# Kernel tuning notes

Measured on AMD Instinct MI355X. Metric: run time of the kernel, lower is better.

The kernel has to match this reference:

```python
import jax, jax.numpy as jnp
import numpy as np

SMOOTHING = 0.9  # NEURON_CONFIG['signal_smoothing']
NUM_SOURCE = 16384
NUM_TARGET = 16384
NUM_BRANCHES = 64
BATCH = 32


def setup_inputs() -> dict:
    key = jax.random.key(0)
    k1, k2, k3, k4 = jax.random.split(key, 4)
    spikes = jax.random.normal(k1, (BATCH, NUM_SOURCE), dtype=jnp.float32)
    attenuation = jax.random.uniform(k2, (NUM_SOURCE, NUM_BRANCHES), dtype=jnp.float32)
    target_indices = jax.random.randint(k3, (NUM_SOURCE, NUM_BRANCHES), 0, NUM_TARGET)
    delays = jax.random.randint(k4, (NUM_SOURCE, NUM_BRANCHES), 0, 6)
    return {"spikes": spikes, "attenuation": attenuation,
            "target_indices": target_indices, "delays": delays}


def reference(spikes, attenuation, target_indices, delays):
    # spikes: [B, S]; attenuation/delays/target_indices: [S, Br]
    B = spikes.shape[0]
    num_target = NUM_TARGET
    att = jnp.clip(attenuation, 0.0, 1.0)
    decay = SMOOTHING ** delays.astype(spikes.dtype)          # [S, Br]
    # fused elementwise: signal per (batch, source, branch)
    signals = spikes[:, :, None] * (att * decay)[None, :, :]   # [B, S, Br]
    flat_t = target_indices.reshape(-1)                        # [S*Br]
    flat_s = signals.reshape(B, -1)                            # [B, S*Br]
    out = jnp.zeros((B, num_target), dtype=spikes.dtype)
    out = out.at[jnp.arange(B)[:, None], flat_t[None, :]].add(flat_s)
    return out
```

## Files before the change

### kernel.cpp

```cpp
#include <hip/hip_runtime.h>

#define S_   16384
#define T_   16384
#define B_   32
#define NEDGES (S_ * 64)
#define GP_  512
#define EPG  2048
#define NBKT 512
#define TPB  32
#define CAP_SRT   2560
#define CAP_STASH 512

__device__ __forceinline__ float edge_weight(float a, int d) {
  float w = fminf(fmaxf(a, 0.0f), 1.0f);
  float r = (d & 1) ? 0.9f : 1.0f;
  r = (d & 2) ? r * 0.81f   : r;
  r = (d & 4) ? r * 0.6561f : r;
  return w * r;
}

__global__ __launch_bounds__(512) void produce(
    const float* __restrict__ spikes,
    const float* __restrict__ att,
    const int*   __restrict__ tgt,
    const int*   __restrict__ del,
    float*        __restrict__ spikesT,
    int2*         __restrict__ rec,
    unsigned int* __restrict__ ofse) {
  __shared__ float tile[32][33];
  __shared__ int4  sbuf4[EPG / 2];
  __shared__ int   cnt5[NBKT], cur5[NBKT], sofs5[NBKT];
  __shared__ int   wtot[8];
  int2* buf = (int2*)sbuf4;

  const int g   = blockIdx.x;
  const int tid = threadIdx.x;
  cnt5[tid] = 0;

  const int s0 = g * 32;
  {
    const int x = tid & 31, y = tid >> 5;
    tile[x][y]      = spikes[(size_t)y        * S_ + s0 + x];
    tile[x][y + 16] = spikes[(size_t)(y + 16) * S_ + s0 + x];
  }

  const int e4  = g * 512 + tid;
  int4   t = reinterpret_cast<const int4*>(tgt)[e4];
  float4 a = reinterpret_cast<const float4*>(att)[e4];
  int4   d = reinterpret_cast<const int4*>(del)[e4];
  const int src = e4 >> 4;

  __syncthreads();

  {
    const int b = tid & 31, j = tid >> 5;
    spikesT[(size_t)(s0 + j)      * 32 + b] = tile[j][b];
    spikesT[(size_t)(s0 + j + 16) * 32 + b] = tile[j + 16][b];
  }

  const int bk0 = t.x >> 5, bk1 = t.y >> 5, bk2 = t.z >> 5, bk3 = t.w >> 5;
  __hip_atomic_fetch_add(&cnt5[bk0], 1, __ATOMIC_RELAXED, __HIP_MEMORY_SCOPE_WORKGROUP);
  __hip_atomic_fetch_add(&cnt5[bk1], 1, __ATOMIC_RELAXED, __HIP_MEMORY_SCOPE_WORKGROUP);
  __hip_atomic_fetch_add(&cnt5[bk2], 1, __ATOMIC_RELAXED, __HIP_MEMORY_SCOPE_WORKGROUP);
  __hip_atomic_fetch_add(&cnt5[bk3], 1, __ATOMIC_RELAXED, __HIP_MEMORY_SCOPE_WORKGROUP);
  __syncthreads();

  int v = cnt5[tid];
  int incl = v;
#pragma unroll
  for (int off = 1; off < 64; off <<= 1) {
    int u = __shfl_up(incl, off);
    if ((tid & 63) >= off) incl += u;
  }
  if ((tid & 63) == 63) wtot[tid >> 6] = incl;
  __syncthreads();
  {
    int base = 0;
    const int wv = tid >> 6;
    for (int i = 0; i < wv; ++i) base += wtot[i];
    const int start = base + incl - v;
    sofs5[tid] = start;
    cur5[tid]  = start;
  }
  __syncthreads();

#define PUT(BK, TL, AV, DV)                                                   \
  {                                                                           \
    int p = __hip_atomic_fetch_add(&cur5[BK], 1, __ATOMIC_RELAXED,            \
                                   __HIP_MEMORY_SCOPE_WORKGROUP);             \
    buf[p] = make_int2(((TL) << 14) | src,                                    \
                       __float_as_int(edge_weight((AV), (DV))));              \
  }
  PUT(bk0, t.x & 31, a.x, d.x)
  PUT(bk1, t.y & 31, a.y, d.y)
  PUT(bk2, t.z & 31, a.z, d.z)
  PUT(bk3, t.w & 31, a.w, d.w)
#undef PUT
  __syncthreads();

  int4* recO = reinterpret_cast<int4*>(rec) + (size_t)g * (EPG / 2);
  recO[tid]       = sbuf4[tid];
  recO[tid + 512] = sbuf4[tid + 512];
  ofse[(size_t)g * NBKT + tid] =
      ((unsigned)cur5[tid] << 16) | (unsigned)sofs5[tid];
}

__global__ __launch_bounds__(256) void transpose_ofse(
    const unsigned int* __restrict__ in, unsigned int* __restrict__ out) {
  __shared__ unsigned tl[32][33];
  const int x = threadIdx.x, y = threadIdx.y;
  const int r0 = blockIdx.y * 32, c0 = blockIdx.x * 32;
  for (int i = y; i < 32; i += 8)
    tl[i][x] = in[(size_t)(r0 + i) * NBKT + c0 + x];
  __syncthreads();
  for (int i = y; i < 32; i += 8)
    out[(size_t)(c0 + i) * GP_ + r0 + x] = tl[x][i];
}

__global__ __launch_bounds__(512) void consume(
    const int2*  __restrict__ rec,
    const unsigned int* __restrict__ ofseT,
    const float* __restrict__ spikesT,
    float* __restrict__ out) {
  __shared__ int2  srt[CAP_SRT];
  __shared__ int2  stash[CAP_STASH];
  __shared__ float otile[TPB][33];
  __shared__ unsigned sse[GP_];
  __shared__ int   h32[TPB], ofs[TPB + 1], cur32[TPB];
  __shared__ int   stash_n;

  const int k   = blockIdx.x;
  const int tid = threadIdx.x;
  const int b   = tid & 31;
  const int hw  = tid >> 5;
  const int sub = (b >> 3);
  const int j   = b & 7;

  if (tid < TPB) h32[tid] = 0;
  if (tid == 0)  stash_n = 0;
  sse[tid] = ofseT[(size_t)k * GP_ + tid];
  __syncthreads();

  int2 rr[8];
  int  rv = 0;
#pragma unroll
  for (int it = 0; it < 8; ++it) {
    const int g = it * 64 + hw * 4 + sub;
    const unsigned u = sse[g];
    const int st = (int)(u & 0xFFFF);
    const int n  = (int)(u >> 16) - st;
    const int2* slice = rec + (size_t)g * EPG + st;
    if (j < n) {
      int2 r = slice[j];
      __hip_atomic_fetch_add(&h32[(r.x >> 14) & 31], 1, __ATOMIC_RELAXED,
                             __HIP_MEMORY_SCOPE_WORKGROUP);
      rr[it] = r;
      rv |= 1 << it;
    }
    for (int j2 = j + 8; j2 < n; j2 += 8) {
      int2 r = slice[j2];
      __hip_atomic_fetch_add(&h32[(r.x >> 14) & 31], 1, __ATOMIC_RELAXED,
                             __HIP_MEMORY_SCOPE_WORKGROUP);
      int sp = __hip_atomic_fetch_add(&stash_n, 1, __ATOMIC_RELAXED,
                                      __HIP_MEMORY_SCOPE_WORKGROUP);
      if (sp < CAP_STASH) stash[sp] = r;
    }
  }
  __syncthreads();

  if (tid < 32) {
    int vv = h32[tid], ii = vv;
#pragma unroll
    for (int off = 1; off < 32; off <<= 1) {
      int uu = __shfl_up(ii, off);
      if (tid >= off) ii += uu;
    }
    ofs[tid]   = ii - vv;
    cur32[tid] = ii - vv;
    if (tid == 31) ofs[32] = ii;
  }
  __syncthreads();

#pragma unroll
  for (int it = 0; it < 8; ++it)
    if (rv & (1 << it)) {
      int2 r = rr[it];
      int p = __hip_atomic_fetch_add(&cur32[(r.x >> 14) & 31], 1,
                                     __ATOMIC_RELAXED,
                                     __HIP_MEMORY_SCOPE_WORKGROUP);
      if (p < CAP_SRT) srt[p] = r;
    }
  const int ns = min(stash_n, CAP_STASH);
  for (int i = tid; i < ns; i += 512) {
    int2 r = stash[i];
    int p = __hip_atomic_fetch_add(&cur32[(r.x >> 14) & 31], 1,
                                   __ATOMIC_RELAXED,
                                   __HIP_MEMORY_SCOPE_WORKGROUP);
    if (p < CAP_SRT) srt[p] = r;
  }
  __syncthreads();

  float acc0 = 0.f, acc1 = 0.f;
  {
    int e        = ofs[hw];
    const int e1 = min(ofs[hw + 1], CAP_SRT);
    for (; e + 4 <= e1; e += 4) {
      int2 r0 = srt[e], r1 = srt[e + 1], r2 = srt[e + 2], r3 = srt[e + 3];
      float s0 = spikesT[(size_t)(r0.x & 0x3FFF) * 32 + b];
      float s1 = spikesT[(size_t)(r1.x & 0x3FFF) * 32 + b];
      float s2 = spikesT[(size_t)(r2.x & 0x3FFF) * 32 + b];
      float s3 = spikesT[(size_t)(r3.x & 0x3FFF) * 32 + b];
      acc0 = fmaf(__int_as_float(r0.y), s0, acc0);
      acc0 = fmaf(__int_as_float(r1.y), s1, acc0);
      acc0 = fmaf(__int_as_float(r2.y), s2, acc0);
      acc0 = fmaf(__int_as_float(r3.y), s3, acc0);
    }
    for (; e < e1; ++e) {
      int2 r = srt[e];
      acc0 = fmaf(__int_as_float(r.y), spikesT[(size_t)(r.x & 0x3FFF) * 32 + b], acc0);
    }
  }
  {
    int e        = ofs[hw + 16];
    const int e1 = min(ofs[hw + 17], CAP_SRT);
    for (; e + 4 <= e1; e += 4) {
      int2 r0 = srt[e], r1 = srt[e + 1], r2 = srt[e + 2], r3 = srt[e + 3];
      float s0 = spikesT[(size_t)(r0.x & 0x3FFF) * 32 + b];
      float s1 = spikesT[(size_t)(r1.x & 0x3FFF) * 32 + b];
      float s2 = spikesT[(size_t)(r2.x & 0x3FFF) * 32 + b];
      float s3 = spikesT[(size_t)(r3.x & 0x3FFF) * 32 + b];
      acc1 = fmaf(__int_as_float(r0.y), s0, acc1);
      acc1 = fmaf(__int_as_float(r1.y), s1, acc1);
      acc1 = fmaf(__int_as_float(r2.y), s2, acc1);
      acc1 = fmaf(__int_as_float(r3.y), s3, acc1);
    }
    for (; e < e1; ++e) {
      int2 r = srt[e];
      acc1 = fmaf(__int_as_float(r.y), spikesT[(size_t)(r.x & 0x3FFF) * 32 + b], acc1);
    }
  }

  otile[hw][b]      = acc0;
  otile[hw + 16][b] = acc1;
  __syncthreads();
  const int bb = tid >> 4;
  const int cc = (tid & 15) * 2;
  float2 o2 = make_float2(otile[cc][bb], otile[cc + 1][bb]);
  *reinterpret_cast<float2*>(&out[(size_t)bb * T_ + k * 32 + cc]) = o2;
}

__global__ void zero_floats(float* __restrict__ p, int n) {
  int i = blockIdx.x * blockDim.x + threadIdx.x;
  if (i < n) p[i] = 0.0f;
}

__global__ void naive_kernel(const float* __restrict__ spikes,
                             const float* __restrict__ att,
                             const int*   __restrict__ tgt,
                             const int*   __restrict__ del,
                             float*       __restrict__ out) {
  int i = blockIdx.x * blockDim.x + threadIdx.x;
  if (i >= NEDGES) return;
  int   s = i >> 6;
  int   t = tgt[i];
  float w = edge_weight(att[i], del[i]);
  for (int b = 0; b < B_; ++b)
    unsafeAtomicAdd(&out[(size_t)b * T_ + t], w * spikes[(size_t)b * S_ + s]);
}

extern "C" void kernel_launch(void* const* d_in, const int* in_sizes, int n_in,
                              void* d_out, int out_size, void* d_ws, size_t ws_size,
                              hipStream_t stream) {
  const float* spikes = (const float*)d_in[0];
  const float* att    = (const float*)d_in[1];
  const int*   tgt    = (const int*)d_in[2];
  const int*   del    = (const int*)d_in[3];
  float*       out    = (float*)d_out;

  const size_t spikesT_bytes = (size_t)S_ * B_ * sizeof(float);
  const size_t rec_bytes     = (size_t)NEDGES * sizeof(int2);
  const size_t ofse_bytes    = (size_t)GP_ * NBKT * sizeof(unsigned);
  const size_t need = spikesT_bytes + rec_bytes + 2 * ofse_bytes + 64;

  if (ws_size < need) {
    zero_floats<<<(B_ * T_ + 255) / 256, 256, 0, stream>>>(out, B_ * T_);
    naive_kernel<<<(NEDGES + 255) / 256, 256, 0, stream>>>(spikes, att, tgt, del, out);
    return;
  }

  char* p = (char*)d_ws;
  float*        spikesT = (float*)p;        p += spikesT_bytes;
  int2*         rec     = (int2*)p;         p += rec_bytes;
  unsigned int* ofse    = (unsigned int*)p; p += ofse_bytes;
  unsigned int* ofseT   = (unsigned int*)p;

  produce<<<GP_, 512, 0, stream>>>(spikes, att, tgt, del, spikesT, rec, ofse);
  transpose_ofse<<<dim3(NBKT / 32, GP_ / 32), dim3(32, 8), 0, stream>>>(ofse, ofseT);
  consume<<<NBKT, 512, 0, stream>>>(rec, ofseT, spikesT, out);
}
```

Measured before the change: 94.21 us.

## Replace consume-side local sort with shared-memory atomic accumulation, drop transpose kernel

The consume kernel no longer builds a per-target histogram, prefix sum and local sort of records before accumulating. Each wavefront now walks its producer-group slices and adds weight*spike products directly into a shared 32x33 accumulator with LDS float atomics. The separate transpose kernel is removed, and consume reads the offset table with strided loads instead. This removes a kernel launch, two sort passes and several barriers, but relies on LDS float atomics, which can contend when edges in a wave share a target. It also serialises each slice's records per wave instead of spreading them across lanes.

After: 251.6 us. 2.67x slower.

```diff
diff --git a/kernel.cpp b/kernel.cpp
--- a/kernel.cpp
+++ b/kernel.cpp
@@ -8,8 +8,6 @@
 #define EPG  2048
 #define NBKT 512
 #define TPB  32
-#define CAP_SRT   2560
-#define CAP_STASH 512
 
 __device__ __forceinline__ float edge_weight(float a, int d) {
   float w = fminf(fmaxf(a, 0.0f), 1.0f);
@@ -105,147 +103,41 @@
       ((unsigned)cur5[tid] << 16) | (unsigned)sofs5[tid];
 }
 
-__global__ __launch_bounds__(256) void transpose_ofse(
-    const unsigned int* __restrict__ in, unsigned int* __restrict__ out) {
-  __shared__ unsigned tl[32][33];
-  const int x = threadIdx.x, y = threadIdx.y;
-  const int r0 = blockIdx.y * 32, c0 = blockIdx.x * 32;
-  for (int i = y; i < 32; i += 8)
-    tl[i][x] = in[(size_t)(r0 + i) * NBKT + c0 + x];
-  __syncthreads();
-  for (int i = y; i < 32; i += 8)
-    out[(size_t)(c0 + i) * GP_ + r0 + x] = tl[x][i];
-}
-
 __global__ __launch_bounds__(512) void consume(
     const int2*  __restrict__ rec,
-    const unsigned int* __restrict__ ofseT,
+    const unsigned int* __restrict__ ofse,
     const float* __restrict__ spikesT,
     float* __restrict__ out) {
-  __shared__ int2  srt[CAP_SRT];
-  __shared__ int2  stash[CAP_STASH];
-  __shared__ float otile[TPB][33];
+  __shared__ float acc[TPB][33];
   __shared__ unsigned sse[GP_];
-  __shared__ int   h32[TPB], ofs[TPB + 1], cur32[TPB];
-  __shared__ int   stash_n;
 
   const int k   = blockIdx.x;
   const int tid = threadIdx.x;
   const int b   = tid & 31;
   const int hw  = tid >> 5;
-  const int sub = (b >> 3);
-  const int j   = b & 7;
 
-  if (tid < TPB) h32[tid] = 0;
-  if (tid == 0)  stash_n = 0;
-  sse[tid] = ofseT[(size_t)k * GP_ + tid];
+  for (int i = tid; i < TPB * 33; i += 512) ((float*)acc)[i] = 0.0f;
+  sse[tid] = ofse[(size_t)tid * NBKT + k];
   __syncthreads();
 
-  int2 rr[8];
-  int  rv = 0;
-#pragma unroll
-  for (int it = 0; it < 8; ++it) {
-    const int g = it * 64 + hw * 4 + sub;
+  for (int it = 0; it < 32; ++it) {
+    const int g = hw + it * 16;
     const unsigned u = sse[g];
     const int st = (int)(u & 0xFFFF);
     const int n  = (int)(u >> 16) - st;
     const int2* slice = rec + (size_t)g * EPG + st;
-    if (j < n) {
-      int2 r = slice[j];
-      __hip_atomic_fetch_add(&h32[(r.x >> 14) & 31], 1, __ATOMIC_RELAXED,
-                             __HIP_MEMORY_SCOPE_WORKGROUP);
-      rr[it] = r;
-      rv |= 1 << it;
-    }
-    for (int j2 = j + 8; j2 < n; j2 += 8) {
-      int2 r = slice[j2];
-      __hip_atomic_fetch_add(&h32[(r.x >> 14) & 31], 1, __ATOMIC_RELAXED,
-                             __HIP_MEMORY_SCOPE_WORKGROUP);
-      int sp = __hip_atomic_fetch_add(&stash_n, 1, __ATOMIC_RELAXED,
-                                      __HIP_MEMORY_SCOPE_WORKGROUP);
-      if (sp < CAP_STASH) stash[sp] = r;
+    for (int j = 0; j < n; ++j) {
+      const int2 r = slice[j];
+      const float v = __int_as_float(r.y) *
+                      spikesT[(size_t)(r.x & 0x3FFF) * 32 + b];
+      atomicAdd(&acc[(r.x >> 14) & 31][b], v);
     }
   }
   __syncthreads();
 
-  if (tid < 32) {
-    int vv = h32[tid], ii = vv;
-#pragma unroll
-    for (int off = 1; off < 32; off <<= 1) {
-      int uu = __shfl_up(ii, off);
-      if (tid >= off) ii += uu;
-    }
-    ofs[tid]   = ii - vv;
-    cur32[tid] = ii - vv;
-    if (tid == 31) ofs[32] = ii;
-  }
-  __syncthreads();
-
-#pragma unroll
-  for (int it = 0; it < 8; ++it)
-    if (rv & (1 << it)) {
-      int2 r = rr[it];
-      int p = __hip_atomic_fetch_add(&cur32[(r.x >> 14) & 31], 1,
-                                     __ATOMIC_RELAXED,
-                                     __HIP_MEMORY_SCOPE_WORKGROUP);
-      if (p < CAP_SRT) srt[p] = r;
-    }
-  const int ns = min(stash_n, CAP_STASH);
-  for (int i = tid; i < ns; i += 512) {
-    int2 r = stash[i];
-    int p = __hip_atomic_fetch_add(&cur32[(r.x >> 14) & 31], 1,
-                                   __ATOMIC_RELAXED,
-                                   __HIP_MEMORY_SCOPE_WORKGROUP);
-    if (p < CAP_SRT) srt[p] = r;
-  }
-  __syncthreads();
-
-  float acc0 = 0.f, acc1 = 0.f;
-  {
-    int e        = ofs[hw];
-    const int e1 = min(ofs[hw + 1], CAP_SRT);
-    for (; e + 4 <= e1; e += 4) {
-      int2 r0 = srt[e], r1 = srt[e + 1], r2 = srt[e + 2], r3 = srt[e + 3];
-      float s0 = spikesT[(size_t)(r0.x & 0x3FFF) * 32 + b];
-      float s1 = spikesT[(size_t)(r1.x & 0x3FFF) * 32 + b];
-      float s2 = spikesT[(size_t)(r2.x & 0x3FFF) * 32 + b];
-      float s3 = spikesT[(size_t)(r3.x & 0x3FFF) * 32 + b];
-      acc0 = fmaf(__int_as_float(r0.y), s0, acc0);
-      acc0 = fmaf(__int_as_float(r1.y), s1, acc0);
-      acc0 = fmaf(__int_as_float(r2.y), s2, acc0);
-      acc0 = fmaf(__int_as_float(r3.y), s3, acc0);
-    }
-    for (; e < e1; ++e) {
-      int2 r = srt[e];
-      acc0 = fmaf(__int_as_float(r.y), spikesT[(size_t)(r.x & 0x3FFF) * 32 + b], acc0);
-    }
-  }
-  {
-    int e        = ofs[hw + 16];
-    const int e1 = min(ofs[hw + 17], CAP_SRT);
-    for (; e + 4 <= e1; e += 4) {
-      int2 r0 = srt[e], r1 = srt[e + 1], r2 = srt[e + 2], r3 = srt[e + 3];
-      float s0 = spikesT[(size_t)(r0.x & 0x3FFF) * 32 + b];
-      float s1 = spikesT[(size_t)(r1.x & 0x3FFF) * 32 + b];
-      float s2 = spikesT[(size_t)(r2.x & 0x3FFF) * 32 + b];
-      float s3 = spikesT[(size_t)(r3.x & 0x3FFF) * 32 + b];
-      acc1 = fmaf(__int_as_float(r0.y), s0, acc1);
-      acc1 = fmaf(__int_as_float(r1.y), s1, acc1);
-      acc1 = fmaf(__int_as_float(r2.y), s2, acc1);
-      acc1 = fmaf(__int_as_float(r3.y), s3, acc1);
-    }
-    for (; e < e1; ++e) {
-      int2 r = srt[e];
-      acc1 = fmaf(__int_as_float(r.y), spikesT[(size_t)(r.x & 0x3FFF) * 32 + b], acc1);
-    }
-  }
-
-  otile[hw][b]      = acc0;
-  otile[hw + 16][b] = acc1;
-  __syncthreads();
   const int bb = tid >> 4;
   const int cc = (tid & 15) * 2;
-  float2 o2 = make_float2(otile[cc][bb], otile[cc + 1][bb]);
+  float2 o2 = make_float2(acc[cc][bb], acc[cc + 1][bb]);
   *reinterpret_cast<float2*>(&out[(size_t)bb * T_ + k * 32 + cc]) = o2;
 }
 
@@ -280,7 +172,7 @@
   const size_t spikesT_bytes = (size_t)S_ * B_ * sizeof(float);
   const size_t rec_bytes     = (size_t)NEDGES * sizeof(int2);
   const size_t ofse_bytes    = (size_t)GP_ * NBKT * sizeof(unsigned);
-  const size_t need = spikesT_bytes + rec_bytes + 2 * ofse_bytes + 64;
+  const size_t need = spikesT_bytes + rec_bytes + ofse_bytes + 64;
 
   if (ws_size < need) {
     zero_floats<<<(B_ * T_ + 255) / 256, 256, 0, stream>>>(out, B_ * T_);
@@ -291,10 +183,8 @@
   char* p = (char*)d_ws;
   float*        spikesT = (float*)p;        p += spikesT_bytes;
   int2*         rec     = (int2*)p;         p += rec_bytes;
-  unsigned int* ofse    = (unsigned int*)p; p += ofse_bytes;
-  unsigned int* ofseT   = (unsigned int*)p;
+  unsigned int* ofse    = (unsigned int*)p;
 
   produce<<<GP_, 512, 0, stream>>>(spikes, att, tgt, del, spikesT, rec, ofse);
-  transpose_ofse<<<dim3(NBKT / 32, GP_ / 32), dim3(32, 8), 0, stream>>>(ofse, ofseT);
-  consume<<<NBKT, 512, 0, stream>>>(rec, ofseT, spikesT, out);
+  consume<<<NBKT, 512, 0, stream>>>(rec, ofse, spikesT, out);
 }
```
